# Kernel optimization log

Hardware: AMD Instinct MI355X
Metric: run time of the kernel (lower is better)

The kernel has to match this reference:

```python
import jax, jax.numpy as jnp
import numpy as np

N, E, IN, OUT, ED, NT, H = 20000, 640000, 128, 256, 32, 16, 8
GATC = OUT // 2          # 128 per-layer GAT width
C = GATC // H            # 16 per-head dim
GINEC = OUT - GATC       # 128


def setup_inputs() -> dict:
    key = jax.random.key(0)
    ks = jax.random.split(key, 16)
    s = 0.05
    return {
        "x": jax.random.normal(ks[0], (N, IN), jnp.float32),
        "edge_index": jax.random.randint(ks[1], (2, E), 0, N, jnp.int64),
        "edge_attr": jax.random.normal(ks[2], (E, ED), jnp.float32),
        "edge_types": jax.random.randint(ks[3], (E,), 0, NT, jnp.int64),
        "gat_W": jax.random.normal(ks[4], (IN, H * C), jnp.float32) * s,
        "gat_b": jnp.zeros((H * C,), jnp.float32),
        "gat_edge_W": jax.random.normal(ks[5], (ED, H * C), jnp.float32) * s,
        "gat_a_src": jax.random.normal(ks[6], (H, C), jnp.float32) * s,
        "gat_a_dst": jax.random.normal(ks[7], (H, C), jnp.float32) * s,
        "gat_a_edge": jax.random.normal(ks[8], (H, C), jnp.float32) * s,
        "gat_type_emb": jax.random.normal(ks[9], (NT, ED), jnp.float32) * s,
        "gine_type_emb": jax.random.normal(ks[10], (NT, ED), jnp.float32) * s,
        "gine_edge_W": jax.random.normal(ks[11], (ED, IN), jnp.float32) * s,
        "gine_edge_b": jnp.zeros((IN,), jnp.float32),
        "gine_eps": jnp.zeros((1,), jnp.float32),
        "gine_W1": jax.random.normal(ks[12], (IN, GINEC), jnp.float32) * s,
        "gine_b1": jnp.zeros((GINEC,), jnp.float32),
        "gine_W2": jax.random.normal(ks[13], (GINEC, GINEC), jnp.float32) * s,
        "gine_b2": jnp.zeros((GINEC,), jnp.float32),
        "comb_W": jax.random.normal(ks[14], (H * C + GINEC, OUT), jnp.float32) * s,
        "comb_b": jnp.zeros((OUT,), jnp.float32),
        "ln_g": jnp.ones((OUT,), jnp.float32),
        "ln_b": jnp.zeros((OUT,), jnp.float32),
    }


def reference(x, edge_index, edge_attr, edge_types,
              gat_W, gat_b, gat_edge_W, gat_a_src, gat_a_dst, gat_a_edge,
              gat_type_emb, gine_type_emb, gine_edge_W, gine_edge_b, gine_eps,
              gine_W1, gine_b1, gine_W2, gine_b2, comb_W, comb_b, ln_g, ln_b):
    n = x.shape[0]
    h_, c_ = gat_a_src.shape
    src, dst = edge_index[0], edge_index[1]

    # ---- GAT branch (edge-featured multi-head attention) ----
    e = edge_attr + gat_type_emb[edge_types]                      # [E, ED]
    h = (x @ gat_W).reshape(n, h_, c_)                            # [N, H, C]
    ee = (e @ gat_edge_W).reshape(-1, h_, c_)                     # [E, H, C]
    a_s = jnp.einsum('nhc,hc->nh', h, gat_a_src)                  # [N, H]
    a_d = jnp.einsum('nhc,hc->nh', h, gat_a_dst)
    a_e = jnp.einsum('ehc,hc->eh', ee, gat_a_edge)                # [E, H]
    logit = jax.nn.leaky_relu(a_s[src] + a_d[dst] + a_e, 0.2)     # [E, H]
    # segment softmax over incoming edges of each destination node
    mx = jax.ops.segment_max(logit, dst, num_segments=n)
    p = jnp.exp(logit - mx[dst])
    denom = jax.ops.segment_sum(p, dst, num_segments=n)
    alpha = p / (denom[dst] + 1e-16)                              # [E, H]
    msg = alpha[:, :, None] * h[src]                              # [E, H, C]
    gat_out = jax.ops.segment_sum(msg, dst, num_segments=n).reshape(n, h_ * c_) + gat_b

    # ---- GINE branch ----
    ep = (edge_attr + gine_type_emb[edge_types]) @ gine_edge_W + gine_edge_b  # [E, IN]
    agg = jax.ops.segment_sum(jax.nn.relu(x[src] + ep), dst, num_segments=n)
    h2 = (1.0 + gine_eps[0]) * x + agg
    gine_out = jax.nn.relu(h2 @ gine_W1 + gine_b1) @ gine_W2 + gine_b2        # [N, GINEC]

    # ---- fuse: Linear + LayerNorm + ReLU (dropout is identity in eval) ----
    z = jnp.concatenate([gat_out, gine_out], axis=-1) @ comb_W + comb_b       # [N, OUT]
    mu = jnp.mean(z, axis=-1, keepdims=True)
    var = jnp.var(z, axis=-1, keepdims=True)
    z = (z - mu) * jax.lax.rsqrt(var + 1e-5) * ln_g + ln_b
    return jax.nn.relu(z)
```

## Files before the change

### kernel.cpp

```cpp
#include <hip/hip_runtime.h>

#define N_NODES 20000
#define N_EDGES 640000

typedef _Float16 h2v   __attribute__((ext_vector_type(2)));
typedef _Float16 h16x8 __attribute__((ext_vector_type(8)));
typedef float    f32x4v __attribute__((ext_vector_type(4)));
typedef unsigned u32x4v __attribute__((ext_vector_type(4)));

__device__ __forceinline__ unsigned packh2(float a, float b){
    h2v v; v.x = (_Float16)a; v.y = (_Float16)b;
    return __builtin_bit_cast(unsigned, v);
}

__global__ void k0_zero(float4* __restrict__ p, int n4){
    int i = blockIdx.x*blockDim.x + threadIdx.x;
    int stride = gridDim.x*blockDim.x;
    float4 z; z.x=0.f; z.y=0.f; z.z=0.f; z.w=0.f;
    for (; i<n4; i+=stride) p[i] = z;
}

__global__ void kD_detect(const int* __restrict__ eidx_w, const int* __restrict__ ety_w,
                          int* __restrict__ flags){
    int i = blockIdx.x*blockDim.x + threadIdx.x;
    int stride = gridDim.x*blockDim.x;
    int a0 = 0, a1 = 0;
    for (int w = 2*i+1; w < 2*N_EDGES; w += 2*stride) a0 |= eidx_w[w];
    for (int w = 2*i+1; w < N_EDGES;   w += 2*stride) a1 |= ety_w[w];
    if (a0) atomicOr(&flags[0], 1);
    if (a1) atomicOr(&flags[1], 1);
}

__global__ void kN_norm(const int* __restrict__ eidx_w, const int* __restrict__ ety_w,
                        const int* __restrict__ flags,
                        int* __restrict__ dst, int* __restrict__ srcty,
                        int* __restrict__ cnt){
    int i = blockIdx.x*blockDim.x + threadIdx.x;
    int stride = gridDim.x*blockDim.x;
    const bool e32 = (flags[0] != 0);
    const bool t32 = (flags[1] != 0);
    for (int e = i; e < N_EDGES; e += stride){
        int s, d, t;
        if (e32){ s = eidx_w[e];   d = eidx_w[N_EDGES + e]; }
        else    { s = eidx_w[2*e]; d = eidx_w[2*N_EDGES + 2*e]; }
        t = t32 ? ety_w[e] : ety_w[2*e];
        s = min(max(s, 0), N_NODES-1);
        d = min(max(d, 0), N_NODES-1);
        t = min(max(t, 0), 15);
        dst[e] = d; srcty[e] = s | (t << 20);
        atomicAdd(&cnt[d], 1);
    }
}

__global__ __launch_bounds__(1024) void kS_scan(const int* __restrict__ cnt,
                                                int* __restrict__ row_ptr,
                                                int* __restrict__ cursor){
    __shared__ int sW[16];
    __shared__ int sWS[16];
    __shared__ int sbase;
    const int t = threadIdx.x, lane = t & 63, wv = t >> 6;
    if (t==0) sbase = 0;
    __syncthreads();
    for (int base=0; base<N_NODES; base+=4096){
        const int idx0 = base + t*4;
        int v0 = (idx0  <N_NODES) ? cnt[idx0  ] : 0;
        int v1 = (idx0+1<N_NODES) ? cnt[idx0+1] : 0;
        int v2 = (idx0+2<N_NODES) ? cnt[idx0+2] : 0;
        int v3 = (idx0+3<N_NODES) ? cnt[idx0+3] : 0;
        int p1 = v0+v1, p2 = p1+v2, tot = p2+v3;
        int xs = tot;
        #pragma unroll
        for (int off=1; off<64; off<<=1){
            int y = __shfl_up(xs, off, 64);
            if (lane >= off) xs += y;
        }
        if (lane==63) sW[wv] = xs;
        __syncthreads();
        if (t < 16){
            int wvv = sW[t], ws = wvv;
            #pragma unroll
            for (int off=1; off<16; off<<=1){
                int y = __shfl_up(ws, off, 16);
                if ((t&15) >= off) ws += y;
            }
            sWS[t] = ws - wvv;
        }
        __syncthreads();
        int ex = sbase + sWS[wv] + xs - tot;
        if (idx0  <N_NODES){ row_ptr[idx0  ]=ex;    cursor[idx0  ]=ex;    }
        if (idx0+1<N_NODES){ row_ptr[idx0+1]=ex+v0; cursor[idx0+1]=ex+v0; }
        if (idx0+2<N_NODES){ row_ptr[idx0+2]=ex+p1; cursor[idx0+2]=ex+p1; }
        if (idx0+3<N_NODES){ row_ptr[idx0+3]=ex+p2; cursor[idx0+3]=ex+p2; }
        __syncthreads();
        if (t==0) sbase += sWS[15] + sW[15];
        __syncthreads();
    }
    if (t==0) row_ptr[N_NODES] = sbase;
}

__global__ __launch_bounds__(256) void kPre(const float* __restrict__ gat_edge_W,
                                            const float* __restrict__ a_edge,
                                            const float* __restrict__ gat_emb,
                                            const float* __restrict__ gine_emb,
                                            const float* __restrict__ gine_edge_W,
                                            const float* __restrict__ gine_edge_b,
                                            float* __restrict__ Mt, float* __restrict__ ATw,
                                            float* __restrict__ Tw){
    const int t = threadIdx.x;
    if (blockIdx.x < 16){
        if (t < 128){
            const int tyv = blockIdx.x;
            float acc = gine_edge_b[t];
            #pragma unroll
            for (int d=0;d<32;d++) acc += gine_emb[tyv*32+d]*gine_edge_W[d*128+t];
            Tw[tyv*128+t] = acc;
        }
        return;
    }
    __shared__ float sM[32*8];
    const int d = t>>3, hh = t&7;
    float acc = 0.f;
    #pragma unroll
    for (int c=0;c<16;c++) acc += gat_edge_W[d*128 + hh*16 + c]*a_edge[hh*16 + c];
    sM[d*8+hh] = acc; Mt[hh*32 + d] = acc;
    __syncthreads();
    if (t < 128){
        int tyv = t>>3, h2 = t&7;
        float a = 0.f;
        #pragma unroll
        for (int dd=0;dd<32;dd++) a += gat_emb[tyv*32+dd]*sM[dd*8+h2];
        ATw[tyv*8+h2] = a;
    }
}

__global__ __launch_bounds__(256) void kW_pack(
    const float* __restrict__ W1, const float* __restrict__ W2,
    const float* __restrict__ combW,
    unsigned* __restrict__ W1p, unsigned* __restrict__ W2p, unsigned* __restrict__ combp)
{
    const int tid = blockIdx.x*256 + threadIdx.x;
    const int chunk = tid >> 6;
    const int l = tid & 63;
    const int n = l & 15, g = l >> 4;
    const float* W; unsigned* P; int NCH, cbase;
    if (chunk < 32)      { W = W1;    P = W1p;   NCH = 128; cbase = chunk; }
    else if (chunk < 64) { W = W2;    P = W2p;   NCH = 128; cbase = chunk - 32; }
    else if (chunk < 192){ W = combW; P = combp; NCH = 256; cbase = chunk - 64; }
    else return;
    const int nblocks = NCH/16;
    const int kstep = cbase / nblocks, nblk = cbase % nblocks;
    const int k0 = kstep*32 + 8*g, col = nblk*16 + n;
    unsigned u0 = packh2(W[(size_t)(k0+0)*NCH + col], W[(size_t)(k0+1)*NCH + col]);
    unsigned u1 = packh2(W[(size_t)(k0+2)*NCH + col], W[(size_t)(k0+3)*NCH + col]);
    unsigned u2 = packh2(W[(size_t)(k0+4)*NCH + col], W[(size_t)(k0+5)*NCH + col]);
    unsigned u3 = packh2(W[(size_t)(k0+6)*NCH + col], W[(size_t)(k0+7)*NCH + col]);
    ((uint4*)P)[(size_t)cbase*64 + l] = make_uint4(u0,u1,u2,u3);
}

__global__ __launch_bounds__(128) void k1_node_prep(
    const float* __restrict__ x, const float* __restrict__ gat_W,
    const float* __restrict__ a_src, const float* __restrict__ a_dst,
    unsigned* __restrict__ xhb, float* __restrict__ as_out, float* __restrict__ ad_out)
{
    __shared__ float sX[8][128];
    __shared__ float sH[128];
    const int t = threadIdx.x;
    const int base = blockIdx.x*8;
    const float4* xin = (const float4*)(x + (size_t)base*128);
    float4* sx4 = (float4*)&sX[0][0];
    for (int i=t;i<256;i+=128) sx4[i] = xin[i];
    __syncthreads();
    float acc[8] = {0,0,0,0,0,0,0,0};
    for (int k=0;k<128;k++){
        float w = gat_W[k*128 + t];
        #pragma unroll
        for (int nn=0;nn<8;nn++) acc[nn] += sX[nn][k]*w;
    }
    const float asv = a_src[t], advv = a_dst[t];
    #pragma unroll
    for (int nn=0;nn<8;nn++){
        const int n = base + nn;
        float vs = acc[nn]*asv, vd = acc[nn]*advv;
        #pragma unroll
        for (int off=8; off>=1; off>>=1){ vs += __shfl_xor(vs,off,16); vd += __shfl_xor(vd,off,16); }
        if ((t&15)==0){ as_out[n*8 + (t>>4)] = vs; ad_out[n*8 + (t>>4)] = vd; }
        __syncthreads();
        sH[t] = acc[nn];
        __syncthreads();
        if (t < 64){
            xhb[(size_t)n*128 + t] = packh2(sX[nn][2*t], sX[nn][2*t+1]);
        } else {
            int i = t - 64;
            xhb[(size_t)n*128 + 64 + i] = packh2(sH[2*i], sH[2*i+1]);
        }
    }
}

__global__ __launch_bounds__(256) void kCE_edge(
    const float* __restrict__ eattr,
    const int* __restrict__ dstA, const int* __restrict__ styA,
    const float* __restrict__ a_s, const float* __restrict__ a_d,
    const float* __restrict__ Mt, const float* __restrict__ ATw,
    const float* __restrict__ gine_emb,
    int* __restrict__ cursor,
    unsigned* __restrict__ evb, float* __restrict__ p_s, int* __restrict__ sty_s)
{
    __shared__ float sEv[32][36];
    __shared__ float sMt[8][36];
    __shared__ float sAT[16*8];
    __shared__ int sPos[32];
    const int t = threadIdx.x;
    sMt[t>>5][t&31] = Mt[t];
    if (t < 128) sAT[t] = ATw[t];
    const int et = t>>3, q = t&7;
    for (int base = blockIdx.x*32; base < N_EDGES; base += gridDim.x*32){
        __syncthreads();
        const int e = base + et;
        float4 f = ((const float4*)eattr)[(size_t)e*8 + q];
        *(float4*)&sEv[et][q*4] = f;
        const int d = dstA[e];
        const int sty = styA[e];
        if (q==0) sPos[et] = atomicAdd(&cursor[d], 1);
        __syncthreads();
        const int pos = sPos[et];
        const int srcn = sty & 0xFFFFF;
        const int tyv = ((unsigned)sty)>>20;
        const float4 ge = ((const float4*)gine_emb)[tyv*8 + q];
        ((uint2*)evb)[(size_t)pos*8 + q] =
            make_uint2(packh2(f.x+ge.x, f.y+ge.y), packh2(f.z+ge.z, f.w+ge.w));
        float acc = 0.f;
        #pragma unroll
        for (int m=0;m<8;m++){
            float4 ev4 = *(const float4*)&sEv[et][m*4];
            float4 m4  = *(const float4*)&sMt[q][m*4];
            acc += ev4.x*m4.x + ev4.y*m4.y + ev4.z*m4.z + ev4.w*m4.w;
        }
        float lg = a_s[srcn*8+q] + a_d[d*8+q] + acc + sAT[tyv*8+q];
        lg = (lg>0.f) ? lg : 0.2f*lg;
        p_s[(size_t)pos*8 + q] = __expf(lg);
        if (q==0) sty_s[pos] = sty;
    }
}

template<bool MASK>
__device__ __forceinline__ void gine_block16(
    int pos0, int rem, int m, int g,
    const unsigned* __restrict__ xhb, const unsigned* __restrict__ evb,
    const float* __restrict__ p_s, const int* __restrict__ sty_s,
    const h16x8* aw, const float* bb,
    float* accA, float* accG, float* ps)
{
    const int mc = MASK ? (m < rem ? m : rem - 1) : m;
    u32x4v uu = ((const u32x4v*)evb)[(size_t)(pos0 + mc)*4 + g];
    h16x8 evf = __builtin_bit_cast(h16x8, uu);

    const _Float16* xp[4];
    int ecl[4];
    #pragma unroll
    for (int r=0;r<4;r++){
        const int er = 4*g + r;
        const int ec = MASK ? (er < rem ? er : rem - 1) : er;
        ecl[r] = pos0 + ec;
        const int srcn = sty_s[pos0 + ec] & 0xFFFFF;
        xp[r] = (const _Float16*)(xhb + (size_t)srcn*128) + m;
    }
    #pragma unroll
    for (int hf4=0; hf4<2; hf4++){
        f32x4v pv[4];
        #pragma unroll
        for (int r=0;r<4;r++){
            pv[r] = *(const f32x4v*)(p_s + (size_t)ecl[r]*8 + hf4*4);
            if (MASK && (4*g + r) >= rem) pv[r] = (f32x4v){0.f,0.f,0.f,0.f};
        }
        #pragma unroll
        for (int r=0;r<4;r++){
            ps[hf4*4+0] += pv[r][0]; ps[hf4*4+1] += pv[r][1];
            ps[hf4*4+2] += pv[r][2]; ps[hf4*4+3] += pv[r][3];
        }
        #pragma unroll
        for (int cc=0; cc<4; cc++){
            const int c = hf4*4 + cc;
            f32x4v Dv = { bb[c], bb[c], bb[c], bb[c] };
            Dv = __builtin_amdgcn_mfma_f32_16x16x32_f16(evf, aw[c], Dv, 0, 0, 0);
            #pragma unroll
            for (int r=0;r<4;r++){
                float xf = (float)xp[r][c*16];
                float hf = (float)xp[r][128 + c*16];
                float tmp = fmaxf(xf + Dv[r], 0.f);
                if (MASK && (4*g + r) >= rem) tmp = 0.f;
                accA[c] += tmp;
                accG[c] += pv[r][cc] * hf;
            }
        }
    }
}

__global__ __launch_bounds__(256) void k3_gather(
    const unsigned* __restrict__ xhb, const unsigned* __restrict__ evb,
    const float* __restrict__ p_s, const int* __restrict__ sty_s,
    const int* __restrict__ row_ptr,
    const float* __restrict__ gine_b, const float* __restrict__ gine_W,
    float* __restrict__ agg, float* __restrict__ gacc)
{
    const int t = threadIdx.x;
    const int lane = t & 63;
    const int m = lane & 15;
    const int g = lane >> 4;

    h16x8 aw[8];
    #pragma unroll
    for (int c=0;c<8;c++){
        #pragma unroll
        for (int j=0;j<8;j++)
            aw[c][j] = (_Float16)gine_W[(8*g + j)*128 + c*16 + m];
    }
    float bb[8];
    #pragma unroll
    for (int c=0;c<8;c++) bb[c] = gine_b[c*16 + m];

    const int nwaves = gridDim.x*4;
    for (int d = blockIdx.x*4 + (t>>6); d < N_NODES; d += nwaves){
        const int row = row_ptr[d], end = row_ptr[d+1];
        float accA[8] = {0,0,0,0,0,0,0,0};
        float accG[8] = {0,0,0,0,0,0,0,0};
        float ps[8]   = {0,0,0,0,0,0,0,0};
        const int deg = end - row;
        int pos0 = row;
        const int nfull = deg >> 4;
        for (int b=0;b<nfull;b++, pos0+=16)
            gine_block16<false>(pos0, 16, m, g, xhb, evb, p_s, sty_s, aw, bb, accA, accG, ps);
        const int rem = deg & 15;
        if (rem)
            gine_block16<true>(pos0, rem, m, g, xhb, evb, p_s, sty_s, aw, bb, accA, accG, ps);
        #pragma unroll
        for (int c=0;c<8;c++){
            accA[c] += __shfl_xor(accA[c], 16, 64);
            accA[c] += __shfl_xor(accA[c], 32, 64);
            accG[c] += __shfl_xor(accG[c], 16, 64);
            accG[c] += __shfl_xor(accG[c], 32, 64);
            ps[c]   += __shfl_xor(ps[c],   16, 64);
            ps[c]   += __shfl_xor(ps[c],   32, 64);
        }
        if (g == 0){
            #pragma unroll
            for (int c=0;c<8;c++){
                const float inv = 1.f/(ps[c] + 1e-16f);
                agg [(size_t)d*128 + c*16 + m] = accA[c];
                gacc[(size_t)d*128 + c*16 + m] = accG[c]*inv;
            }
        }
    }
}

#define K4N 32
__global__ __launch_bounds__(256) void k4_final(
    const float* __restrict__ x, const float* __restrict__ agg, const float* __restrict__ gacc,
    const float* __restrict__ gat_b, const float* __restrict__ eps_p,
    const unsigned* __restrict__ W1p, const float* __restrict__ b1,
    const unsigned* __restrict__ W2p, const float* __restrict__ gb2,
    const unsigned* __restrict__ combp, const float* __restrict__ comb_b,
    const float* __restrict__ ln_g, const float* __restrict__ ln_b,
    float* __restrict__ out)
{
    __shared__ _Float16 sHi[K4N][136];
    __shared__ _Float16 sLo[K4N][136];
    __shared__ _Float16 sCH[K4N][264];
    __shared__ float sRed[K4N][8];
    __shared__ float sMV[K4N][2];
    const int t = threadIdx.x;
    const int l = t & 63, wid = t >> 6;
    const int n = l & 15, g = l >> 4;
    const float epsv = 1.f + eps_p[0];
    const int base = blockIdx.x*K4N;

    for (int i = t; i < K4N*32; i += 256){
        const int node = i >> 5, c4 = i & 31;
        float4 xv = ((const float4*)x   )[(size_t)(base+node)*32 + c4];
        float4 av = ((const float4*)agg )[(size_t)(base+node)*32 + c4];
        float4 gv = ((const float4*)gacc)[(size_t)(base+node)*32 + c4];
        float4 bv = ((const float4*)gat_b)[c4];
        float h0 = epsv*xv.x + av.x, h1 = epsv*xv.y + av.y;
        float h2_ = epsv*xv.z + av.z, h3 = epsv*xv.w + av.w;
        _Float16 f0=(_Float16)h0, f1=(_Float16)h1, f2=(_Float16)h2_, f3=(_Float16)h3;
        h2v p01; p01.x=f0; p01.y=f1;  h2v p23; p23.x=f2; p23.y=f3;
        *(uint2*)&sHi[node][c4*4] = make_uint2(__builtin_bit_cast(unsigned,p01),
                                               __builtin_bit_cast(unsigned,p23));
        h2v q01, q23;
        q01.x=(_Float16)(h0-(float)f0); q01.y=(_Float16)(h1-(float)f1);
        q23.x=(_Float16)(h2_-(float)f2); q23.y=(_Float16)(h3-(float)f3);
        *(uint2*)&sLo[node][c4*4] = make_uint2(__builtin_bit_cast(unsigned,q01),
                                               __builtin_bit_cast(unsigned,q23));
        *(uint2*)&sCH[node][c4*4] = make_uint2(packh2(gv.x+bv.x, gv.y+bv.y),
                                               packh2(gv.z+bv.z, gv.w+bv.w));
    }
    __syncthreads();

    f32x4v acc1[2][2];
    #pragma unroll
    for (int mt=0;mt<2;mt++)
        #pragma unroll
        for (int nt=0;nt<2;nt++){
            float b = b1[32*wid + 16*nt + n];
            acc1[mt][nt] = (f32x4v){b,b,b,b};
        }
    #pragma unroll
    for (int ks=0;ks<4;ks++){
        h16x8 bfr[2];
        #pragma unroll
        for (int nt=0;nt<2;nt++){
            uint4 u = ((const uint4*)W1p)[(size_t)((ks*8 + 2*wid + nt)*64 + l)];
            bfr[nt] = __builtin_bit_cast(h16x8, u);
        }
        #pragma unroll
        for (int mt=0;mt<2;mt++){
            const int row = 16*mt + n;
            h16x8 ahi = *(const h16x8*)&sHi[row][8*g + 32*ks];
            h16x8 alo = *(const h16x8*)&sLo[row][8*g + 32*ks];
            #pragma unroll
            for (int nt=0;nt<2;nt++){
                acc1[mt][nt] = __builtin_amdgcn_mfma_f32_16x16x32_f16(ahi, bfr[nt], acc1[mt][nt], 0,0,0);
                acc1[mt][nt] = __builtin_amdgcn_mfma_f32_16x16x32_f16(alo, bfr[nt], acc1[mt][nt], 0,0,0);
            }
        }
    }
    __syncthreads();
    #pragma unroll
    for (int mt=0;mt<2;mt++)
        #pragma unroll
        for (int nt=0;nt<2;nt++)
            #pragma unroll
            for (int r=0;r<4;r++)
                sHi[16*mt + 4*g + r][32*wid + 16*nt + n] = (_Float16)fmaxf(acc1[mt][nt][r], 0.f);
    __syncthreads();

    f32x4v acc2[2][2];
    #pragma unroll
    for (int mt=0;mt<2;mt++)
        #pragma unroll
        for (int nt=0;nt<2;nt++){
            float b = gb2[32*wid + 16*nt + n];
            acc2[mt][nt] = (f32x4v){b,b,b,b};
        }
    #pragma unroll
    for (int ks=0;ks<4;ks++){
        h16x8 bfr[2];
        #pragma unroll
        for (int nt=0;nt<2;nt++){
            uint4 u = ((const uint4*)W2p)[(size_t)((ks*8 + 2*wid + nt)*64 + l)];
            bfr[nt] = __builtin_bit_cast(h16x8, u);
        }
        #pragma unroll
        for (int mt=0;mt<2;mt++){
            h16x8 a = *(const h16x8*)&sHi[16*mt + n][8*g + 32*ks];
            #pragma unroll
            for (int nt=0;nt<2;nt++)
                acc2[mt][nt] = __builtin_amdgcn_mfma_f32_16x16x32_f16(a, bfr[nt], acc2[mt][nt], 0,0,0);
        }
    }
    #pragma unroll
    for (int mt=0;mt<2;mt++)
        #pragma unroll
        for (int nt=0;nt<2;nt++)
            #pragma unroll
            for (int r=0;r<4;r++)
                sCH[16*mt + 4*g + r][128 + 32*wid + 16*nt + n] = (_Float16)acc2[mt][nt][r];
    __syncthreads();

    f32x4v accC[2][4];
    #pragma unroll
    for (int mt=0;mt<2;mt++)
        #pragma unroll
        for (int nt=0;nt<4;nt++){
            float b = comb_b[64*wid + 16*nt + n];
            accC[mt][nt] = (f32x4v){b,b,b,b};
        }
    #pragma unroll
    for (int ks=0;ks<8;ks++){
        h16x8 bfr[4];
        #pragma unroll
        for (int nt=0;nt<4;nt++){
            uint4 u = ((const uint4*)combp)[(size_t)((ks*16 + 4*wid + nt)*64 + l)];
            bfr[nt] = __builtin_bit_cast(h16x8, u);
        }
        #pragma unroll
        for (int mt=0;mt<2;mt++){
            h16x8 a = *(const h16x8*)&sCH[16*mt + n][8*g + 32*ks];
            #pragma unroll
            for (int nt=0;nt<4;nt++)
                accC[mt][nt] = __builtin_amdgcn_mfma_f32_16x16x32_f16(a, bfr[nt], accC[mt][nt], 0,0,0);
        }
    }

    #pragma unroll
    for (int mt=0;mt<2;mt++)
        #pragma unroll
        for (int r=0;r<4;r++){
            float s1=0.f, s2=0.f;
            #pragma unroll
            for (int nt=0;nt<4;nt++){ float z = accC[mt][nt][r]; s1 += z; s2 += z*z; }
            #pragma unroll
            for (int off=1; off<16; off<<=1){ s1 += __shfl_xor(s1,off,16); s2 += __shfl_xor(s2,off,16); }
            if (n==0){
                sRed[16*mt + 4*g + r][2*wid  ] = s1;
                sRed[16*mt + 4*g + r][2*wid+1] = s2;
            }
        }
    __syncthreads();
    if (t < K4N){
        float a1 = sRed[t][0]+sRed[t][2]+sRed[t][4]+sRed[t][6];
        float a2 = sRed[t][1]+sRed[t][3]+sRed[t][5]+sRed[t][7];
        float mu = a1*(1.f/256.f);
        float var = a2*(1.f/256.f) - mu*mu;
        sMV[t][0] = mu; sMV[t][1] = rsqrtf(var + 1e-5f);
    }
    __syncthreads();
    float lg[4], lb[4];
    #pragma unroll
    for (int nt=0;nt<4;nt++){ int ch = 64*wid + 16*nt + n; lg[nt]=ln_g[ch]; lb[nt]=ln_b[ch]; }
    #pragma unroll
    for (int mt=0;mt<2;mt++)
        #pragma unroll
        for (int r=0;r<4;r++){
            const int row = 16*mt + 4*g + r;
            const float mu = sMV[row][0], rs = sMV[row][1];
            #pragma unroll
            for (int nt=0;nt<4;nt++){
                const int ch = 64*wid + 16*nt + n;
                float zz = accC[mt][nt][r];
                out[(size_t)(base+row)*256 + ch] = fmaxf((zz-mu)*rs*lg[nt] + lb[nt], 0.f);
            }
        }
}

extern "C" void kernel_launch(void* const* d_in, const int* in_sizes, int n_in,
                              void* d_out, int out_size, void* d_ws, size_t ws_size,
                              hipStream_t stream)
{
    (void)in_sizes; (void)n_in; (void)out_size; (void)ws_size;
    const float* x           = (const float*)d_in[0];
    const int*   eidx_w      = (const int*)  d_in[1];
    const float* eattr       = (const float*)d_in[2];
    const int*   ety_w       = (const int*)  d_in[3];
    const float* gat_W       = (const float*)d_in[4];
    const float* gat_b       = (const float*)d_in[5];
    const float* gat_edge_W  = (const float*)d_in[6];
    const float* a_src       = (const float*)d_in[7];
    const float* a_dst       = (const float*)d_in[8];
    const float* a_edge      = (const float*)d_in[9];
    const float* gat_emb     = (const float*)d_in[10];
    const float* gine_emb    = (const float*)d_in[11];
    const float* gine_edge_W = (const float*)d_in[12];
    const float* gine_edge_b = (const float*)d_in[13];
    const float* gine_eps    = (const float*)d_in[14];
    const float* W1          = (const float*)d_in[15];
    const float* b1          = (const float*)d_in[16];
    const float* W2          = (const float*)d_in[17];
    const float* gb2         = (const float*)d_in[18];
    const float* comb_W      = (const float*)d_in[19];
    const float* comb_b      = (const float*)d_in[20];
    const float* ln_g        = (const float*)d_in[21];
    const float* ln_b        = (const float*)d_in[22];
    float* out = (float*)d_out;

    char* ws = (char*)d_ws;
    size_t off = 0;
    auto alloc = [&](size_t bytes)->void*{ void* p = ws + off; off += (bytes + 255)/256*256; return p; };
    size_t zero_start = off;
    int*      flags  = (int*)     alloc(256);
    int*      cnt    = (int*)     alloc((size_t)N_NODES*4);
    size_t zero_bytes = off - zero_start;
    int*      dstA   = (int*)     alloc((size_t)N_EDGES*4);
    int*      styA   = (int*)     alloc((size_t)N_EDGES*4);
    int*      rowp   = (int*)     alloc((size_t)(N_NODES+1)*4);
    int*      cursor = (int*)     alloc((size_t)N_NODES*4);
    int*      sty_s  = (int*)     alloc((size_t)N_EDGES*4);
    unsigned* evb    = (unsigned*)alloc((size_t)N_EDGES*64);
    float*    p_s    = (float*)   alloc((size_t)N_EDGES*8*4);
    unsigned* xhb    = (unsigned*)alloc((size_t)N_NODES*128*4);
    float*    a_s    = (float*)   alloc((size_t)N_NODES*8*4);
    float*    a_d    = (float*)   alloc((size_t)N_NODES*8*4);
    float*    Mt     = (float*)   alloc(32*8*4);
    float*    ATw    = (float*)   alloc(16*8*4);
    float*    Tw     = (float*)   alloc(16*128*4);
    float*    agg    = (float*)   alloc((size_t)N_NODES*128*4);
    float*    gacc   = (float*)   alloc((size_t)N_NODES*128*4);
    unsigned* W1p    = (unsigned*)alloc((size_t)32*1024);
    unsigned* W2p    = (unsigned*)alloc((size_t)32*1024);
    unsigned* combp  = (unsigned*)alloc((size_t)128*1024);

    int n4 = (int)(zero_bytes/16);
    k0_zero<<<(n4+255)/256, 256, 0, stream>>>((float4*)(ws + zero_start), n4);
    kD_detect<<<512, 256, 0, stream>>>(eidx_w, ety_w, flags);
    kN_norm<<<1024, 256, 0, stream>>>(eidx_w, ety_w, flags, dstA, styA, cnt);
    kS_scan<<<1, 1024, 0, stream>>>(cnt, rowp, cursor);

    kW_pack<<<48, 256, 0, stream>>>(W1, W2, comb_W, W1p, W2p, combp);
    kPre<<<17, 256, 0, stream>>>(gat_edge_W, a_edge, gat_emb, gine_emb,
                                 gine_edge_W, gine_edge_b, Mt, ATw, Tw);
    k1_node_prep<<<N_NODES/8, 128, 0, stream>>>(x, gat_W, a_src, a_dst, xhb, a_s, a_d);

    kCE_edge<<<2500, 256, 0, stream>>>(eattr, dstA, styA, a_s, a_d, Mt, ATw, gine_emb,
                                       cursor, evb, p_s, sty_s);

    k3_gather<<<2500, 256, 0, stream>>>(xhb, evb, p_s, sty_s, rowp,
                                        gine_edge_b, gine_edge_W, agg, gacc);

    k4_final<<<N_NODES/K4N, 256, 0, stream>>>(x, agg, gacc, gat_b, gine_eps,
                                              W1p, b1, W2p, gb2, combp, comb_b,
                                              ln_g, ln_b, out);
}
```

Baseline: 434.7 us.

## Precompute edge ranks, drop shared-memory edge kernel, interleave per-edge records

The counting pass now records each edge's rank within its destination, so the edge kernel computes its CSR slot as row_ptr[d]+rank instead of doing a second atomic on a cursor array. The edge kernel drops shared memory and barriers, keeps the Mt projection in registers and reduces it with lane shuffles. Edge features, attention weights and packed src/type are stored together in one 128-byte record per edge so the gather kernel reads them from one region. The cost is an extra rank array and padding in the record layout, which raises the bytes written per edge.

```diff
diff --git a/kernel.cpp b/kernel.cpp
--- a/kernel.cpp
+++ b/kernel.cpp
@@ -34,7 +34,7 @@
 __global__ void kN_norm(const int* __restrict__ eidx_w, const int* __restrict__ ety_w,
                         const int* __restrict__ flags,
                         int* __restrict__ dst, int* __restrict__ srcty,
-                        int* __restrict__ cnt){
+                        int* __restrict__ rankA, int* __restrict__ cnt){
     int i = blockIdx.x*blockDim.x + threadIdx.x;
     int stride = gridDim.x*blockDim.x;
     const bool e32 = (flags[0] != 0);
@@ -48,13 +48,12 @@
         d = min(max(d, 0), N_NODES-1);
         t = min(max(t, 0), 15);
         dst[e] = d; srcty[e] = s | (t << 20);
-        atomicAdd(&cnt[d], 1);
+        rankA[e] = atomicAdd(&cnt[d], 1);
     }
 }
 
 __global__ __launch_bounds__(1024) void kS_scan(const int* __restrict__ cnt,
-                                                int* __restrict__ row_ptr,
-                                                int* __restrict__ cursor){
+                                                int* __restrict__ row_ptr){
     __shared__ int sW[16];
     __shared__ int sWS[16];
     __shared__ int sbase;
@@ -87,10 +86,10 @@
         }
         __syncthreads();
         int ex = sbase + sWS[wv] + xs - tot;
-        if (idx0  <N_NODES){ row_ptr[idx0  ]=ex;    cursor[idx0  ]=ex;    }
-        if (idx0+1<N_NODES){ row_ptr[idx0+1]=ex+v0; cursor[idx0+1]=ex+v0; }
-        if (idx0+2<N_NODES){ row_ptr[idx0+2]=ex+p1; cursor[idx0+2]=ex+p1; }
-        if (idx0+3<N_NODES){ row_ptr[idx0+3]=ex+p2; cursor[idx0+3]=ex+p2; }
+        if (idx0  <N_NODES){ row_ptr[idx0  ]=ex;    }
+        if (idx0+1<N_NODES){ row_ptr[idx0+1]=ex+v0; }
+        if (idx0+2<N_NODES){ row_ptr[idx0+2]=ex+p1; }
+        if (idx0+3<N_NODES){ row_ptr[idx0+3]=ex+p2; }
         __syncthreads();
         if (t==0) sbase += sWS[15] + sW[15];
         __syncthreads();
@@ -199,59 +198,70 @@
 __global__ __launch_bounds__(256) void kCE_edge(
     const float* __restrict__ eattr,
     const int* __restrict__ dstA, const int* __restrict__ styA,
+    const int* __restrict__ rankA, const int* __restrict__ rowp,
     const float* __restrict__ a_s, const float* __restrict__ a_d,
     const float* __restrict__ Mt, const float* __restrict__ ATw,
     const float* __restrict__ gine_emb,
-    int* __restrict__ cursor,
-    unsigned* __restrict__ evb, float* __restrict__ p_s, int* __restrict__ sty_s)
+    unsigned* __restrict__ erec)
 {
-    __shared__ float sEv[32][36];
-    __shared__ float sMt[8][36];
-    __shared__ float sAT[16*8];
-    __shared__ int sPos[32];
     const int t = threadIdx.x;
-    sMt[t>>5][t&31] = Mt[t];
-    if (t < 128) sAT[t] = ATw[t];
-    const int et = t>>3, q = t&7;
-    for (int base = blockIdx.x*32; base < N_EDGES; base += gridDim.x*32){
-        __syncthreads();
-        const int e = base + et;
+    const int q = t & 7;
+    float4 mtr[8];
+    #pragma unroll
+    for (int h=0;h<8;h++) mtr[h] = ((const float4*)Mt)[h*8 + q];
+
+    const int e0 = (blockIdx.x*256 + t) >> 3;
+    const int estride = (gridDim.x*256) >> 3;
+    for (int e = e0; e < N_EDGES; e += estride){
         float4 f = ((const float4*)eattr)[(size_t)e*8 + q];
-        *(float4*)&sEv[et][q*4] = f;
-        const int d = dstA[e];
-        const int sty = styA[e];
-        if (q==0) sPos[et] = atomicAdd(&cursor[d], 1);
-        __syncthreads();
-        const int pos = sPos[et];
+        const int d    = dstA[e];
+        const int sty  = styA[e];
+        const int pos  = rowp[d] + rankA[e];
         const int srcn = sty & 0xFFFFF;
-        const int tyv = ((unsigned)sty)>>20;
+        const int tyv  = ((unsigned)sty)>>20;
+
         const float4 ge = ((const float4*)gine_emb)[tyv*8 + q];
-        ((uint2*)evb)[(size_t)pos*8 + q] =
+        ((uint2*)erec)[(size_t)pos*16 + q] =
             make_uint2(packh2(f.x+ge.x, f.y+ge.y), packh2(f.z+ge.z, f.w+ge.w));
-        float acc = 0.f;
-        #pragma unroll
-        for (int m=0;m<8;m++){
-            float4 ev4 = *(const float4*)&sEv[et][m*4];
-            float4 m4  = *(const float4*)&sMt[q][m*4];
-            acc += ev4.x*m4.x + ev4.y*m4.y + ev4.z*m4.z + ev4.w*m4.w;
-        }
-        float lg = a_s[srcn*8+q] + a_d[d*8+q] + acc + sAT[tyv*8+q];
+
+        float ph[8];
+        #pragma unroll
+        for (int h=0;h<8;h++)
+            ph[h] = f.x*mtr[h].x + f.y*mtr[h].y + f.z*mtr[h].z + f.w*mtr[h].w;
+        #pragma unroll
+        for (int i=0;i<4;i++){
+            float send = (q&1) ? ph[2*i] : ph[2*i+1];
+            float recv = __shfl_xor(send, 1, 64);
+            ph[i] = ((q&1) ? ph[2*i+1] : ph[2*i]) + recv;
+        }
+        #pragma unroll
+        for (int i=0;i<2;i++){
+            float send = (q&2) ? ph[2*i] : ph[2*i+1];
+            float recv = __shfl_xor(send, 2, 64);
+            ph[i] = ((q&2) ? ph[2*i+1] : ph[2*i]) + recv;
+        }
+        {
+            float send = (q&4) ? ph[0] : ph[1];
+            float recv = __shfl_xor(send, 4, 64);
+            ph[0] = ((q&4) ? ph[1] : ph[0]) + recv;
+        }
+
+        float lg = a_s[srcn*8+q] + a_d[d*8+q] + ph[0] + ATw[tyv*8+q];
         lg = (lg>0.f) ? lg : 0.2f*lg;
-        p_s[(size_t)pos*8 + q] = __expf(lg);
-        if (q==0) sty_s[pos] = sty;
+        ((float*)erec)[(size_t)pos*32 + 16 + q] = __expf(lg);
+        ((int*)erec)[(size_t)pos*32 + 24 + q] = sty;
     }
 }
 
 template<bool MASK>
 __device__ __forceinline__ void gine_block16(
     int pos0, int rem, int m, int g,
-    const unsigned* __restrict__ xhb, const unsigned* __restrict__ evb,
-    const float* __restrict__ p_s, const int* __restrict__ sty_s,
+    const unsigned* __restrict__ xhb, const unsigned* __restrict__ erec,
     const h16x8* aw, const float* bb,
     float* accA, float* accG, float* ps)
 {
     const int mc = MASK ? (m < rem ? m : rem - 1) : m;
-    u32x4v uu = ((const u32x4v*)evb)[(size_t)(pos0 + mc)*4 + g];
+    u32x4v uu = ((const u32x4v*)erec)[(size_t)(pos0 + mc)*8 + g];
     h16x8 evf = __builtin_bit_cast(h16x8, uu);
 
     const _Float16* xp[4];
@@ -261,7 +271,7 @@
         const int er = 4*g + r;
         const int ec = MASK ? (er < rem ? er : rem - 1) : er;
         ecl[r] = pos0 + ec;
-        const int srcn = sty_s[pos0 + ec] & 0xFFFFF;
+        const int srcn = ((const int*)erec)[(size_t)(pos0 + ec)*32 + 24] & 0xFFFFF;
         xp[r] = (const _Float16*)(xhb + (size_t)srcn*128) + m;
     }
     #pragma unroll
@@ -269,7 +279,7 @@
         f32x4v pv[4];
         #pragma unroll
         for (int r=0;r<4;r++){
-            pv[r] = *(const f32x4v*)(p_s + (size_t)ecl[r]*8 + hf4*4);
+            pv[r] = *(const f32x4v*)((const float*)erec + (size_t)ecl[r]*32 + 16 + hf4*4);
             if (MASK && (4*g + r) >= rem) pv[r] = (f32x4v){0.f,0.f,0.f,0.f};
         }
         #pragma unroll
@@ -296,8 +306,7 @@
 }
 
 __global__ __launch_bounds__(256) void k3_gather(
-    const unsigned* __restrict__ xhb, const unsigned* __restrict__ evb,
-    const float* __restrict__ p_s, const int* __restrict__ sty_s,
+    const unsigned* __restrict__ xhb, const unsigned* __restrict__ erec,
     const int* __restrict__ row_ptr,
     const float* __restrict__ gine_b, const float* __restrict__ gine_W,
     float* __restrict__ agg, float* __restrict__ gacc)
@@ -328,10 +337,10 @@
         int pos0 = row;
         const int nfull = deg >> 4;
         for (int b=0;b<nfull;b++, pos0+=16)
-            gine_block16<false>(pos0, 16, m, g, xhb, evb, p_s, sty_s, aw, bb, accA, accG, ps);
+            gine_block16<false>(pos0, 16, m, g, xhb, erec, aw, bb, accA, accG, ps);
         const int rem = deg & 15;
         if (rem)
-            gine_block16<true>(pos0, rem, m, g, xhb, evb, p_s, sty_s, aw, bb, accA, accG, ps);
+            gine_block16<true>(pos0, rem, m, g, xhb, erec, aw, bb, accA, accG, ps);
         #pragma unroll
         for (int c=0;c<8;c++){
             accA[c] += __shfl_xor(accA[c], 16, 64);
@@ -571,11 +580,9 @@
     size_t zero_bytes = off - zero_start;
     int*      dstA   = (int*)     alloc((size_t)N_EDGES*4);
     int*      styA   = (int*)     alloc((size_t)N_EDGES*4);
+    int*      rankA  = (int*)     alloc((size_t)N_EDGES*4);
     int*      rowp   = (int*)     alloc((size_t)(N_NODES+1)*4);
-    int*      cursor = (int*)     alloc((size_t)N_NODES*4);
-    int*      sty_s  = (int*)     alloc((size_t)N_EDGES*4);
-    unsigned* evb    = (unsigned*)alloc((size_t)N_EDGES*64);
-    float*    p_s    = (float*)   alloc((size_t)N_EDGES*8*4);
+    unsigned* erec   = (unsigned*)alloc((size_t)N_EDGES*128);
     unsigned* xhb    = (unsigned*)alloc((size_t)N_NODES*128*4);
     float*    a_s    = (float*)   alloc((size_t)N_NODES*8*4);
     float*    a_d    = (float*)   alloc((size_t)N_NODES*8*4);
@@ -591,18 +598,18 @@
     int n4 = (int)(zero_bytes/16);
     k0_zero<<<(n4+255)/256, 256, 0, stream>>>((float4*)(ws + zero_start), n4);
     kD_detect<<<512, 256, 0, stream>>>(eidx_w, ety_w, flags);
-    kN_norm<<<1024, 256, 0, stream>>>(eidx_w, ety_w, flags, dstA, styA, cnt);
-    kS_scan<<<1, 1024, 0, stream>>>(cnt, rowp, cursor);
+    kN_norm<<<1024, 256, 0, stream>>>(eidx_w, ety_w, flags, dstA, styA, rankA, cnt);
+    kS_scan<<<1, 1024, 0, stream>>>(cnt, rowp);
 
     kW_pack<<<48, 256, 0, stream>>>(W1, W2, comb_W, W1p, W2p, combp);
     kPre<<<17, 256, 0, stream>>>(gat_edge_W, a_edge, gat_emb, gine_emb,
                                  gine_edge_W, gine_edge_b, Mt, ATw, Tw);
     k1_node_prep<<<N_NODES/8, 128, 0, stream>>>(x, gat_W, a_src, a_dst, xhb, a_s, a_d);
 
-    kCE_edge<<<2500, 256, 0, stream>>>(eattr, dstA, styA, a_s, a_d, Mt, ATw, gine_emb,
-                                       cursor, evb, p_s, sty_s);
-
-    k3_gather<<<2500, 256, 0, stream>>>(xhb, evb, p_s, sty_s, rowp,
+    kCE_edge<<<2500, 256, 0, stream>>>(eattr, dstA, styA, rankA, rowp,
+                                       a_s, a_d, Mt, ATw, gine_emb, erec);
+
+    k3_gather<<<2500, 256, 0, stream>>>(xhb, erec, rowp,
                                         gine_edge_b, gine_edge_W, agg, gacc);
 
     k4_final<<<N_NODES/K4N, 256, 0, stream>>>(x, agg, gacc, gat_b, gine_eps,
```

Measured after the change: 422.8 us. 2.7% less time.
